# Kernel tuning notes

Hardware: AMD Instinct MI355X
Metric: run time of the kernel (lower is better)

Reference implementation:

```python
import jax, jax.numpy as jnp
import numpy as np

B, T, D = 2, 2048, 1024
H, KVH = 16, 4
HD = D // H            # 64
HALF = HD // 2         # 32
DFF = 4096
KW = 15
EPS = 1e-6


def zcrms(x, scale):
    # zero-centred RMSNorm: (1 + scale) * x / rms(x)
    rms = jnp.sqrt(jnp.mean(jnp.square(x.astype(jnp.float32)), axis=-1, keepdims=True) + EPS)
    return ((1.0 + scale) * x / rms).astype(x.dtype)


def apply_rope(x, cos, sin):
    # x: [B, H, T, HD]; cos/sin: [T, HALF]
    c = cos[None, None, :, :]
    s = sin[None, None, :, :]
    x1, x2 = x[..., :HALF], x[..., HALF:]
    return jnp.concatenate([x1 * c - x2 * s, x2 * c + x1 * s], axis=-1)


def setup_inputs() -> dict:
    key = jax.random.key(0)
    ks = jax.random.split(key, 20)
    std = 0.02
    inp = {
        "x": jax.random.normal(ks[0], (B, T, D), jnp.float32),
        "mask": jnp.ones((1, 1, T, T), dtype=bool),
        "cos": jnp.cos(jnp.arange(T, dtype=jnp.float32)[:, None]
                       * (10000.0 ** (-jnp.arange(HALF, dtype=jnp.float32) / HALF))[None, :]),
        "sin": jnp.sin(jnp.arange(T, dtype=jnp.float32)[:, None]
                       * (10000.0 ** (-jnp.arange(HALF, dtype=jnp.float32) / HALF))[None, :]),
        # attention
        "attn_norm_scale": jax.random.normal(ks[1], (D,), jnp.float32) * std,
        "q_kernel": jax.random.normal(ks[2], (D, D), jnp.float32) * std,
        "k_kernel": jax.random.normal(ks[3], (D, KVH * HD), jnp.float32) * std,
        "v_kernel": jax.random.normal(ks[4], (D, KVH * HD), jnp.float32) * std,
        "q_norm_scale": jax.random.normal(ks[5], (HD,), jnp.float32) * std,
        "k_norm_scale": jax.random.normal(ks[6], (HD,), jnp.float32) * std,
        "o_kernel": jax.random.normal(ks[7], (D, D), jnp.float32) * std,
        # conv module
        "conv_norm_scale": jax.random.normal(ks[8], (D,), jnp.float32) * std,
        "pw_up_kernel": jax.random.normal(ks[9], (D, 2 * D), jnp.float32) * std,
        "dw_kernel": jax.random.normal(ks[10], (KW, 1, D), jnp.float32) * std,
        "conv_inner_norm_scale": jax.random.normal(ks[11], (D,), jnp.float32) * std,
        "pw_down_kernel": jax.random.normal(ks[12], (D, D), jnp.float32) * std,
        # ffn
        "ffn_norm_scale": jax.random.normal(ks[13], (D,), jnp.float32) * std,
        "gate_kernel": jax.random.normal(ks[14], (D, DFF), jnp.float32) * std,
        "up_kernel": jax.random.normal(ks[15], (D, DFF), jnp.float32) * std,
        "down_kernel": jax.random.normal(ks[16], (DFF, D), jnp.float32) * std,
    }
    return inp


def reference(x, mask, cos, sin, attn_norm_scale, q_kernel, k_kernel, v_kernel,
              q_norm_scale, k_norm_scale, o_kernel, conv_norm_scale, pw_up_kernel,
              dw_kernel, conv_inner_norm_scale, pw_down_kernel, ffn_norm_scale,
              gate_kernel, up_kernel, down_kernel):
    # ---- pre-norm self-attention (GQA + QK-RMSNorm + RoPE) ----
    h = zcrms(x, attn_norm_scale)
    q = (h @ q_kernel).reshape(B, T, H, HD).transpose(0, 2, 1, 3)      # [B,H,T,HD]
    k = (h @ k_kernel).reshape(B, T, KVH, HD).transpose(0, 2, 1, 3)    # [B,KVH,T,HD]
    v = (h @ v_kernel).reshape(B, T, KVH, HD).transpose(0, 2, 1, 3)
    q = zcrms(q, q_norm_scale)
    k = zcrms(k, k_norm_scale)
    rep = H // KVH
    k = jnp.repeat(k, rep, axis=1)
    v = jnp.repeat(v, rep, axis=1)
    q = apply_rope(q, cos, sin)
    k = apply_rope(k, cos, sin)
    scale = jnp.sqrt(jnp.float32(HD))
    aw = jnp.einsum('bhqd,bhkd->bhqk', q, k) / scale
    aw = jnp.where(mask, aw, jnp.finfo(aw.dtype).min)
    aw = jax.nn.softmax(aw, axis=-1)
    attn = jnp.einsum('bhqk,bhkd->bhqd', aw, v).transpose(0, 2, 1, 3).reshape(B, T, D)
    x = x + attn @ o_kernel

    # ---- conformer conv module: pw_up -> GLU -> depthwise conv -> norm -> pw_down ----
    h = zcrms(x, conv_norm_scale)
    u = h @ pw_up_kernel
    u1, u2 = jnp.split(u, 2, axis=-1)
    g = u1 * jax.nn.sigmoid(u2)                                        # [B,T,D]
    c = jax.lax.conv_general_dilated(
        g, dw_kernel, window_strides=(1,), padding='SAME',
        feature_group_count=D, dimension_numbers=('NWC', 'WIO', 'NWC'))
    c = zcrms(c, conv_inner_norm_scale)
    x = x + c @ pw_down_kernel

    # ---- gated FFN with drelu activation ----
    h = zcrms(x, ffn_norm_scale)
    ff = jax.nn.relu(h @ gate_kernel) * jax.nn.relu(h @ up_kernel)
    x = x + ff @ down_kernel
    return x
```

## Files before the change

kernel.cpp:

```cpp
#include <hip/hip_runtime.h>


#define TT   2048
#define NTOK 4096

typedef __attribute__((ext_vector_type(8))) short short8;
typedef __attribute__((ext_vector_type(4))) float floatx4;

__device__ __forceinline__ unsigned short f2bf(float f) {
  unsigned int u = __float_as_uint(f);
  u = (u + 0x7fffu + ((u >> 16) & 1u)) >> 16;
  return (unsigned short)u;
}
__device__ __forceinline__ float bf2f(unsigned short s) {
  return __uint_as_float(((unsigned int)s) << 16);
}

__device__ __forceinline__ void glds16(const void* g, void* lds_base) {
  __builtin_amdgcn_global_load_lds(
      (const __attribute__((address_space(1))) void*)g,
      (__attribute__((address_space(3))) void*)lds_base, 16, 0, 0);
}

struct WJobs {
  const float* src[9];
  unsigned short* dst[9];
  int K[9], M[9], pm[9];
  int start[10];
};

__global__ __launch_bounds__(256) void wconv_all_kernel(WJobs tab) {
  int b = blockIdx.x;
  int j = 0;
  while (b >= tab.start[j + 1]) j++;
  int t = b - tab.start[j];
  const float* src = tab.src[j];
  unsigned short* dst = tab.dst[j];
  int K = tab.K[j], M = tab.M[j], pm = tab.pm[j];
  int mt = M >> 5;
  int m0 = (t % mt) * 32, k0 = (t / mt) * 32;
  int rowbase;
  if (pm == 0)      rowbase = m0;
  else if (pm == 1) rowbase = ((m0 & 1023) >> 5) * 64 + (m0 >> 10) * 32;
  else if (pm == 2) rowbase = (m0 >> 5) * 64;
  else              rowbase = (m0 >> 5) * 64 + 32;
  __shared__ float tile[32][33];
  int tx = threadIdx.x & 31, ty = threadIdx.x >> 5;
  for (int r = ty; r < 32; r += 8)
    tile[r][tx] = src[(size_t)(k0 + r) * M + m0 + tx];
  __syncthreads();
  for (int r = ty; r < 32; r += 8)
    dst[(size_t)(rowbase + r) * K + k0 + tx] = f2bf(tile[tx][r]);
}

__global__ __launch_bounds__(256) void rmsnorm_kernel(
    const float* __restrict__ x, const float* __restrict__ scale,
    unsigned short* __restrict__ out) {
  int t = blockIdx.x, tid = threadIdx.x;
  float4 xv = ((const float4*)(x + (size_t)t * 1024))[tid];
  float ss = xv.x * xv.x + xv.y * xv.y + xv.z * xv.z + xv.w * xv.w;
#pragma unroll
  for (int off = 32; off > 0; off >>= 1) ss += __shfl_down(ss, off);
  __shared__ float red[4];
  if ((tid & 63) == 0) red[tid >> 6] = ss;
  __syncthreads();
  float rinv = rsqrtf((red[0] + red[1] + red[2] + red[3]) * (1.0f / 1024.0f) + 1e-6f);
  float4 sv = ((const float4*)scale)[tid];
  ushort4 o;
  o.x = f2bf((1.0f + sv.x) * xv.x * rinv);
  o.y = f2bf((1.0f + sv.y) * xv.y * rinv);
  o.z = f2bf((1.0f + sv.z) * xv.z * rinv);
  o.w = f2bf((1.0f + sv.w) * xv.w * rinv);
  ((ushort4*)(out + (size_t)t * 1024))[tid] = o;
}

template <int BN, int FUSE, bool OUT_BF16, bool RELU, bool RESID>
__global__ __launch_bounds__(256, 2) void gemm_bt_kernel(
    const unsigned short* __restrict__ A, const unsigned short* __restrict__ Bt,
    void* __restrict__ Cout, const float* __restrict__ resid, int K, int M) {
  constexpr int NI = BN / 32;
  __shared__ __align__(16) unsigned short As[128 * 64];
  __shared__ __align__(16) unsigned short Bs[BN * 64];
  const int tid = threadIdx.x;
  const int wid = tid >> 6, lane = tid & 63;
  const int quad = lane >> 4, l16 = lane & 15;
  const int wm = (wid >> 1) * 64, wn = (wid & 1) * (BN / 2);
  const int row0 = blockIdx.y * 128;
  const int col0 = blockIdx.x * BN;

  floatx4 acc[4][NI];
#pragma unroll
  for (int mi = 0; mi < 4; mi++)
#pragma unroll
    for (int ni = 0; ni < NI; ni++) acc[mi][ni] = (floatx4){0.f, 0.f, 0.f, 0.f};

  const unsigned short* Ag = A + (size_t)row0 * K;
  const unsigned short* Bg = Bt + (size_t)col0 * K;

  for (int k0 = 0; k0 < K; k0 += 64) {
#pragma unroll
    for (int j = 0; j < 4; j++) {
      int ci = tid + j * 256;
      int r = ci >> 3, c = (ci & 7) ^ (r & 7);
      glds16(Ag + (size_t)r * K + k0 + c * 8, &As[(wid * 64 + j * 256) * 8]);
    }
#pragma unroll
    for (int j = 0; j < BN / 32; j++) {
      int ci = tid + j * 256;
      int r = ci >> 3, c = (ci & 7) ^ (r & 7);
      glds16(Bg + (size_t)r * K + k0 + c * 8, &Bs[(wid * 64 + j * 256) * 8]);
    }
    __syncthreads();
#pragma unroll
    for (int kk = 0; kk < 64; kk += 32) {
      short8 a[4], b[NI];
#pragma unroll
      for (int mi = 0; mi < 4; mi++) {
        int r = wm + mi * 16 + l16;
        a[mi] = *(const short8*)&As[r * 64 + (((kk >> 3) + quad) ^ (r & 7)) * 8];
      }
#pragma unroll
      for (int ni = 0; ni < NI; ni++) {
        int r = wn + ni * 16 + l16;
        b[ni] = *(const short8*)&Bs[r * 64 + (((kk >> 3) + quad) ^ (r & 7)) * 8];
      }
#pragma unroll
      for (int mi = 0; mi < 4; mi++)
#pragma unroll
        for (int ni = 0; ni < NI; ni++)
          acc[mi][ni] = __builtin_amdgcn_mfma_f32_16x16x32_bf16(a[mi], b[ni], acc[mi][ni], 0, 0, 0);
    }
    __syncthreads();
  }

  if (FUSE == 0) {
#pragma unroll
    for (int mi = 0; mi < 4; mi++) {
#pragma unroll
      for (int reg = 0; reg < 4; reg++) {
        int grow = row0 + wm + mi * 16 + quad * 4 + reg;
#pragma unroll
        for (int ni = 0; ni < NI; ni++) {
          int gcol = col0 + wn + ni * 16 + l16;
          float v = acc[mi][ni][reg];
          if (RESID) v += resid[(size_t)grow * M + gcol];
          if (RELU) v = fmaxf(v, 0.f);
          if (OUT_BF16) ((unsigned short*)Cout)[(size_t)grow * M + gcol] = f2bf(v);
          else          ((float*)Cout)[(size_t)grow * M + gcol] = v;
        }
      }
    }
  } else {
    const int group = (col0 + wn) >> 6;
    const int MW = M >> 1;
#pragma unroll
    for (int mi = 0; mi < 4; mi++) {
#pragma unroll
      for (int reg = 0; reg < 4; reg++) {
        int grow = row0 + wm + mi * 16 + quad * 4 + reg;
#pragma unroll
        for (int ni = 0; ni < NI / 2; ni++) {
          int f = group * 32 + ni * 16 + l16;
          float a = acc[mi][ni][reg], b = acc[mi][ni + NI / 2][reg];
          float v;
          if (FUSE == 1) v = a / (1.0f + __expf(-b));
          else           v = fmaxf(a, 0.f) * fmaxf(b, 0.f);
          ((unsigned short*)Cout)[(size_t)grow * MW + f] = f2bf(v);
        }
      }
    }
  }
}

#define QSCALE 0.180336880111f

__global__ __launch_bounds__(256) void qknorm_rope_kernel(
    const unsigned short* __restrict__ qkv, const float* __restrict__ cosb,
    const float* __restrict__ sinb, const float* __restrict__ qns,
    const float* __restrict__ kns, unsigned short* __restrict__ qb,
    unsigned short* __restrict__ kb, unsigned short* __restrict__ vb) {
  int tok = blockIdx.x;
  int tid = threadIdx.x, w = tid >> 6, lane = tid & 63;
  int pos = tok & (TT - 1);
  int half = lane & 31;
  float c = cosb[pos * 32 + half], s = sinb[pos * 32 + half];
  const unsigned short* row = qkv + (size_t)tok * 1536;
  for (int hr = w; hr < 20; hr += 4) {
    float v = bf2f(row[hr * 64 + lane]);
    float ss = v * v;
#pragma unroll
    for (int off = 32; off > 0; off >>= 1) ss += __shfl_xor(ss, off);
    float rinv = rsqrtf(ss * (1.0f / 64.0f) + 1e-6f);
    float sc = (hr < 16) ? qns[lane] : kns[lane];
    float nv = (1.0f + sc) * v * rinv;
    float partner = __shfl_xor(nv, 32);
    float outv = (lane < 32) ? (nv * c - partner * s) : (nv * c + partner * s);
    if (hr < 16) qb[(size_t)tok * 1024 + hr * 64 + lane] = f2bf(outv * QSCALE);
    else         kb[(size_t)tok * 256 + (hr - 16) * 64 + lane] = f2bf(outv);
  }
  vb[(size_t)tok * 256 + tid] = row[1280 + tid];
}

__global__ __launch_bounds__(256) void vtrans_kernel(
    const unsigned short* __restrict__ vb, unsigned short* __restrict__ vt) {
  __shared__ unsigned short t[64 * 65];
  int ktile = blockIdx.x;
  int g = blockIdx.y;
  int bi = g >> 2, kvh = g & 3;
  int tid = threadIdx.x;
#pragma unroll
  for (int j = 0; j < 2; j++) {
    int ci = tid + j * 256;
    int r = ci >> 3, c8 = (ci & 7) * 8;
    union { uint4 v; unsigned short u[8]; } uu;
    uu.v = *(const uint4*)(vb + (size_t)(bi * TT + ktile * 64 + r) * 256 + kvh * 64 + c8);
#pragma unroll
    for (int e = 0; e < 8; e++) t[r * 65 + c8 + e] = uu.u[e];
  }
  __syncthreads();
#pragma unroll
  for (int j = 0; j < 2; j++) {
    int ci = tid + j * 256;
    int d = ci >> 3, c8 = (ci & 7) * 8;
    union { uint4 v; unsigned short u[8]; } uu;
#pragma unroll
    for (int e = 0; e < 8; e++) uu.u[e] = t[(c8 + e) * 65 + d];
    *(uint4*)(vt + ((size_t)(g * 64 + d)) * TT + ktile * 64 + c8) = uu.v;
  }
}

__global__ __launch_bounds__(256) void flash_kernel(
    const unsigned short* __restrict__ qb, const unsigned short* __restrict__ kb,
    const unsigned short* __restrict__ vt, unsigned short* __restrict__ ob) {
  const int qt = blockIdx.x;
  const int bh = blockIdx.y;
  const int bi = bh >> 4, h = bh & 15, kvh = h >> 2;
  const int tid = threadIdx.x, w = tid >> 6, lane = tid & 63;
  const int quad = lane >> 4, l16 = lane & 15;

  __shared__ __align__(16) unsigned short Ks[2][64 * 64];
  __shared__ __align__(16) unsigned short Vs[2][64 * 64];
  __shared__ __align__(16) unsigned short Ps[128 * 72];

  const unsigned short* qsrc = qb + ((size_t)(bi * TT + qt * 128)) * 1024 + h * 64;
  short8 qf[2][2];
#pragma unroll
  for (int af = 0; af < 2; af++) {
    const unsigned short* qr = qsrc + (size_t)(w * 32 + af * 16 + l16) * 1024;
    qf[af][0] = *(const short8*)(qr + quad * 8);
    qf[af][1] = *(const short8*)(qr + 32 + quad * 8);
  }

  const unsigned short* kbase = kb + ((size_t)(bi * TT)) * 256 + kvh * 64;
  const unsigned short* vbase = vt + ((size_t)(bi * 4 + kvh)) * (64 * TT);

  floatx4 oacc[2][4];
  floatx4 lacc[2];
#pragma unroll
  for (int af = 0; af < 2; af++) {
    lacc[af] = (floatx4){0.f, 0.f, 0.f, 0.f};
#pragma unroll
    for (int di = 0; di < 4; di++) oacc[af][di] = (floatx4){0.f, 0.f, 0.f, 0.f};
  }
  const short8 ones = (short8){0x3F80, 0x3F80, 0x3F80, 0x3F80,
                               0x3F80, 0x3F80, 0x3F80, 0x3F80};

#pragma unroll
  for (int j = 0; j < 2; j++) {
    int ci = tid + j * 256;
    int r = ci >> 3, c = (ci & 7) ^ (r & 7);
    glds16(kbase + (size_t)r * 256 + c * 8, &Ks[0][(w * 64 + j * 256) * 8]);
    glds16(vbase + (size_t)r * TT + c * 8, &Vs[0][(w * 64 + j * 256) * 8]);
  }

  for (int kt = 0; kt < 32; kt++) {
    const int buf = kt & 1;
    __syncthreads();
    if (kt < 31) {
#pragma unroll
      for (int j = 0; j < 2; j++) {
        int ci = tid + j * 256;
        int r = ci >> 3, c = (ci & 7) ^ (r & 7);
        glds16(kbase + (size_t)((kt + 1) * 64 + r) * 256 + c * 8,
               &Ks[buf ^ 1][(w * 64 + j * 256) * 8]);
        glds16(vbase + (size_t)r * TT + (kt + 1) * 64 + c * 8,
               &Vs[buf ^ 1][(w * 64 + j * 256) * 8]);
      }
    }

    short8 kf[4][2];
#pragma unroll
    for (int ni = 0; ni < 4; ni++) {
      int rb = ni * 16 + l16;
      kf[ni][0] = *(const short8*)&Ks[buf][rb * 64 + ((quad ^ (rb & 7)) * 8)];
      kf[ni][1] = *(const short8*)&Ks[buf][rb * 64 + (((4 + quad) ^ (rb & 7)) * 8)];
    }
#pragma unroll
    for (int af = 0; af < 2; af++) {
#pragma unroll
      for (int ni = 0; ni < 4; ni++) {
        floatx4 s = (floatx4){0.f, 0.f, 0.f, 0.f};
        s = __builtin_amdgcn_mfma_f32_16x16x32_bf16(qf[af][0], kf[ni][0], s, 0, 0, 0);
        s = __builtin_amdgcn_mfma_f32_16x16x32_bf16(qf[af][1], kf[ni][1], s, 0, 0, 0);
#pragma unroll
        for (int r = 0; r < 4; r++)
          Ps[(w * 32 + af * 16 + quad * 4 + r) * 72 + ((ni ^ quad) * 16 + l16)] =
              (unsigned short)(__float_as_uint(__builtin_amdgcn_exp2f(s[r])) >> 16);
      }
    }
    short8 vf[4][2];
#pragma unroll
    for (int di = 0; di < 4; di++) {
      int rb = di * 16 + l16;
      vf[di][0] = *(const short8*)&Vs[buf][rb * 64 + ((quad ^ (rb & 7)) * 8)];
      vf[di][1] = *(const short8*)&Vs[buf][rb * 64 + (((4 + quad) ^ (rb & 7)) * 8)];
    }
#pragma unroll
    for (int af = 0; af < 2; af++) {
      const int rr = w * 32 + af * 16 + l16;
      const int sw = l16 >> 2;
      short8 pa0 = *(const short8*)&Ps[rr * 72 + (((quad >> 1) ^ sw) * 16 + (quad & 1) * 8)];
      short8 pa1 = *(const short8*)&Ps[rr * 72 + ((((quad >> 1) + 2) ^ sw) * 16 + (quad & 1) * 8)];
      lacc[af] = __builtin_amdgcn_mfma_f32_16x16x32_bf16(pa0, ones, lacc[af], 0, 0, 0);
      lacc[af] = __builtin_amdgcn_mfma_f32_16x16x32_bf16(pa1, ones, lacc[af], 0, 0, 0);
#pragma unroll
      for (int di = 0; di < 4; di++) {
        oacc[af][di] = __builtin_amdgcn_mfma_f32_16x16x32_bf16(pa0, vf[di][0], oacc[af][di], 0, 0, 0);
        oacc[af][di] = __builtin_amdgcn_mfma_f32_16x16x32_bf16(pa1, vf[di][1], oacc[af][di], 0, 0, 0);
      }
    }
  }

  unsigned short* obase = ob + ((size_t)(bi * TT + qt * 128)) * 1024 + h * 64;
#pragma unroll
  for (int af = 0; af < 2; af++) {
    float rl[4];
#pragma unroll
    for (int r = 0; r < 4; r++) rl[r] = 1.0f / lacc[af][r];
#pragma unroll
    for (int di = 0; di < 4; di++)
#pragma unroll
      for (int r = 0; r < 4; r++) {
        int qrow = w * 32 + af * 16 + quad * 4 + r;
        obase[(size_t)qrow * 1024 + di * 16 + l16] = f2bf(oacc[af][di][r] * rl[r]);
      }
  }
}

__global__ __launch_bounds__(256) void convnorm_kernel(
    const unsigned short* __restrict__ g, const float* __restrict__ dw,
    const float* __restrict__ scale, unsigned short* __restrict__ out) {
  int tok = blockIdx.x;
  int bi = tok >> 11, pos = tok & (TT - 1);
  int tid = threadIdx.x, c0 = tid * 4;
  float a0 = 0.f, a1 = 0.f, a2 = 0.f, a3 = 0.f;
#pragma unroll
  for (int wk = 0; wk < 15; wk++) {
    int pp = pos + wk - 7;
    if (pp < 0 || pp >= TT) continue;
    ushort4 gv = *(const ushort4*)(g + ((size_t)(bi * TT + pp)) * 1024 + c0);
    float4 kv = *(const float4*)(dw + wk * 1024 + c0);
    a0 += bf2f(gv.x) * kv.x;
    a1 += bf2f(gv.y) * kv.y;
    a2 += bf2f(gv.z) * kv.z;
    a3 += bf2f(gv.w) * kv.w;
  }
  float ss = a0 * a0 + a1 * a1 + a2 * a2 + a3 * a3;
#pragma unroll
  for (int off = 32; off > 0; off >>= 1) ss += __shfl_down(ss, off);
  __shared__ float red[4];
  if ((tid & 63) == 0) red[tid >> 6] = ss;
  __syncthreads();
  float rinv = rsqrtf((red[0] + red[1] + red[2] + red[3]) * (1.0f / 1024.0f) + 1e-6f);
  float4 sv = *(const float4*)(scale + c0);
  ushort4 o;
  o.x = f2bf((1.0f + sv.x) * a0 * rinv);
  o.y = f2bf((1.0f + sv.y) * a1 * rinv);
  o.z = f2bf((1.0f + sv.z) * a2 * rinv);
  o.w = f2bf((1.0f + sv.w) * a3 * rinv);
  *(ushort4*)(out + (size_t)tok * 1024 + c0) = o;
}

extern "C" void kernel_launch(void* const* d_in, const int* in_sizes, int n_in,
                              void* d_out, int out_size, void* d_ws, size_t ws_size,
                              hipStream_t stream) {
  const float* x        = (const float*)d_in[0];
  const float* cosb     = (const float*)d_in[2];
  const float* sinb     = (const float*)d_in[3];
  const float* attn_ns  = (const float*)d_in[4];
  const float* qkern    = (const float*)d_in[5];
  const float* kkern    = (const float*)d_in[6];
  const float* vkern    = (const float*)d_in[7];
  const float* qns      = (const float*)d_in[8];
  const float* kns      = (const float*)d_in[9];
  const float* okern    = (const float*)d_in[10];
  const float* conv_ns  = (const float*)d_in[11];
  const float* pwupk    = (const float*)d_in[12];
  const float* dwk      = (const float*)d_in[13];
  const float* convi_ns = (const float*)d_in[14];
  const float* pwdnk    = (const float*)d_in[15];
  const float* ffn_ns   = (const float*)d_in[16];
  const float* gatek    = (const float*)d_in[17];
  const float* upk      = (const float*)d_in[18];
  const float* downk    = (const float*)d_in[19];
  float* out = (float*)d_out;
  char* ws = (char*)d_ws;

  const size_t O_QKVT = 0;
  const size_t O_OT   = O_QKVT + (size_t)1536 * 1024 * 2;
  const size_t O_UPT  = O_OT   + (size_t)1024 * 1024 * 2;
  const size_t O_DNT  = O_UPT  + (size_t)2048 * 1024 * 2;
  const size_t O_GUT  = O_DNT  + (size_t)1024 * 1024 * 2;
  const size_t O_DWNT = O_GUT  + (size_t)8192 * 1024 * 2;
  const size_t O_H    = O_DWNT + (size_t)4096 * 1024 * 2;
  const size_t O_BIG1 = O_H    + (size_t)4096 * 1024 * 2;
  const size_t O_QB   = O_BIG1 + (size_t)4096 * 8192 * 2;
  const size_t O_KB   = O_QB   + (size_t)4096 * 1024 * 2;
  const size_t O_VB   = O_KB   + (size_t)4096 * 256 * 2;
  const size_t O_VT   = O_VB   + (size_t)4096 * 256 * 2;
  const size_t O_ECN  = O_VT   + (size_t)8 * 64 * 2048 * 2;
  const size_t O_X1   = O_ECN  + (size_t)4096 * 1024 * 2;
  const size_t O_X2   = O_X1   + (size_t)4096 * 1024 * 4;
  const size_t O_BIG2 = O_X2   + (size_t)4096 * 1024 * 4;

  unsigned short* qkvT = (unsigned short*)(ws + O_QKVT);
  unsigned short* oT   = (unsigned short*)(ws + O_OT);
  unsigned short* upT  = (unsigned short*)(ws + O_UPT);
  unsigned short* dnT  = (unsigned short*)(ws + O_DNT);
  unsigned short* guT  = (unsigned short*)(ws + O_GUT);
  unsigned short* dwT  = (unsigned short*)(ws + O_DWNT);
  unsigned short* hbuf = (unsigned short*)(ws + O_H);
  unsigned short* big1u = (unsigned short*)(ws + O_BIG1);
  unsigned short* qbuf = (unsigned short*)(ws + O_QB);
  unsigned short* kbuf = (unsigned short*)(ws + O_KB);
  unsigned short* vbuf = (unsigned short*)(ws + O_VB);
  unsigned short* vtb  = (unsigned short*)(ws + O_VT);
  unsigned short* ecn  = (unsigned short*)(ws + O_ECN);
  float*          x1   = (float*)(ws + O_X1);
  float*          x2   = (float*)(ws + O_X2);
  unsigned short* big2 = (unsigned short*)(ws + O_BIG2);

  WJobs tab;
  tab.src[0] = qkern;  tab.dst[0] = qkvT;                       tab.K[0] = 1024; tab.M[0] = 1024; tab.pm[0] = 0;
  tab.src[1] = kkern;  tab.dst[1] = qkvT + (size_t)1024 * 1024; tab.K[1] = 1024; tab.M[1] = 256;  tab.pm[1] = 0;
  tab.src[2] = vkern;  tab.dst[2] = qkvT + (size_t)1280 * 1024; tab.K[2] = 1024; tab.M[2] = 256;  tab.pm[2] = 0;
  tab.src[3] = okern;  tab.dst[3] = oT;                         tab.K[3] = 1024; tab.M[3] = 1024; tab.pm[3] = 0;
  tab.src[4] = pwupk;  tab.dst[4] = upT;                        tab.K[4] = 1024; tab.M[4] = 2048; tab.pm[4] = 1;
  tab.src[5] = pwdnk;  tab.dst[5] = dnT;                        tab.K[5] = 1024; tab.M[5] = 1024; tab.pm[5] = 0;
  tab.src[6] = gatek;  tab.dst[6] = guT;                        tab.K[6] = 1024; tab.M[6] = 4096; tab.pm[6] = 2;
  tab.src[7] = upk;    tab.dst[7] = guT;                        tab.K[7] = 1024; tab.M[7] = 4096; tab.pm[7] = 3;
  tab.src[8] = downk;  tab.dst[8] = dwT;                        tab.K[8] = 4096; tab.M[8] = 1024; tab.pm[8] = 0;
  tab.start[0] = 0;
  for (int i = 0; i < 9; i++)
    tab.start[i + 1] = tab.start[i] + (tab.M[i] >> 5) * (tab.K[i] >> 5);
  wconv_all_kernel<<<tab.start[9], 256, 0, stream>>>(tab);

  rmsnorm_kernel<<<NTOK, 256, 0, stream>>>(x, attn_ns, hbuf);
  gemm_bt_kernel<128, 0, true, false, false><<<dim3(12, 32), 256, 0, stream>>>(
      hbuf, qkvT, big1u, nullptr, 1024, 1536);
  qknorm_rope_kernel<<<NTOK, 256, 0, stream>>>(big1u, cosb, sinb, qns, kns,
                                               qbuf, kbuf, vbuf);
  vtrans_kernel<<<dim3(32, 8), 256, 0, stream>>>(vbuf, vtb);
  flash_kernel<<<dim3(16, 32), 256, 0, stream>>>(qbuf, kbuf, vtb, ecn);
  gemm_bt_kernel<64, 0, false, false, true><<<dim3(16, 32), 256, 0, stream>>>(
      ecn, oT, x1, x, 1024, 1024);

  rmsnorm_kernel<<<NTOK, 256, 0, stream>>>(x1, conv_ns, hbuf);
  gemm_bt_kernel<128, 1, false, false, false><<<dim3(16, 32), 256, 0, stream>>>(
      hbuf, upT, big2, nullptr, 1024, 2048);
  convnorm_kernel<<<NTOK, 256, 0, stream>>>(big2, dwk, convi_ns, ecn);
  gemm_bt_kernel<64, 0, false, false, true><<<dim3(16, 32), 256, 0, stream>>>(
      ecn, dnT, x2, x1, 1024, 1024);

  rmsnorm_kernel<<<NTOK, 256, 0, stream>>>(x2, ffn_ns, hbuf);
  gemm_bt_kernel<128, 2, false, false, false><<<dim3(64, 32), 256, 0, stream>>>(
      hbuf, guT, big1u, nullptr, 1024, 8192);
  gemm_bt_kernel<64, 0, false, false, true><<<dim3(16, 32), 256, 0, stream>>>(
      big1u, dwT, out, x2, 4096, 1024);
}
```

Baseline: 484.9 us.

## Store residual stream in bf16, read V directly, and double flash block size

Intermediate residual activations x1 and x2 are now stored as bf16 instead of fp32. The rmsnorm and GEMM epilogues are templated to read bf16 input or residual, which halves that traffic at a precision cost. The separate V copy out of the QKV buffer is removed, and vtrans now reads V directly from the QKV output. The flash attention kernel moves to 512 threads and 256-row query tiles with a new XOR-swizzled P layout, so each K/V tile is shared by more queries. The grid shrinks from 512 to 256 blocks, which may reduce occupancy.

```diff
diff --git a/kernel.cpp b/kernel.cpp
--- a/kernel.cpp
+++ b/kernel.cpp
@@ -53,12 +53,20 @@
     dst[(size_t)(rowbase + r) * K + k0 + tx] = f2bf(tile[tx][r]);
 }
 
+template <bool BF16IN>
 __global__ __launch_bounds__(256) void rmsnorm_kernel(
-    const float* __restrict__ x, const float* __restrict__ scale,
+    const void* __restrict__ xin, const float* __restrict__ scale,
     unsigned short* __restrict__ out) {
   int t = blockIdx.x, tid = threadIdx.x;
-  float4 xv = ((const float4*)(x + (size_t)t * 1024))[tid];
-  float ss = xv.x * xv.x + xv.y * xv.y + xv.z * xv.z + xv.w * xv.w;
+  float xv[4];
+  if (BF16IN) {
+    ushort4 u = ((const ushort4*)((const unsigned short*)xin + (size_t)t * 1024))[tid];
+    xv[0] = bf2f(u.x); xv[1] = bf2f(u.y); xv[2] = bf2f(u.z); xv[3] = bf2f(u.w);
+  } else {
+    float4 u = ((const float4*)((const float*)xin + (size_t)t * 1024))[tid];
+    xv[0] = u.x; xv[1] = u.y; xv[2] = u.z; xv[3] = u.w;
+  }
+  float ss = xv[0] * xv[0] + xv[1] * xv[1] + xv[2] * xv[2] + xv[3] * xv[3];
 #pragma unroll
   for (int off = 32; off > 0; off >>= 1) ss += __shfl_down(ss, off);
   __shared__ float red[4];
@@ -67,17 +75,17 @@
   float rinv = rsqrtf((red[0] + red[1] + red[2] + red[3]) * (1.0f / 1024.0f) + 1e-6f);
   float4 sv = ((const float4*)scale)[tid];
   ushort4 o;
-  o.x = f2bf((1.0f + sv.x) * xv.x * rinv);
-  o.y = f2bf((1.0f + sv.y) * xv.y * rinv);
-  o.z = f2bf((1.0f + sv.z) * xv.z * rinv);
-  o.w = f2bf((1.0f + sv.w) * xv.w * rinv);
+  o.x = f2bf((1.0f + sv.x) * xv[0] * rinv);
+  o.y = f2bf((1.0f + sv.y) * xv[1] * rinv);
+  o.z = f2bf((1.0f + sv.z) * xv[2] * rinv);
+  o.w = f2bf((1.0f + sv.w) * xv[3] * rinv);
   ((ushort4*)(out + (size_t)t * 1024))[tid] = o;
 }
 
-template <int BN, int FUSE, bool OUT_BF16, bool RELU, bool RESID>
+template <int BN, int FUSE, int OUT, int RES>
 __global__ __launch_bounds__(256, 2) void gemm_bt_kernel(
     const unsigned short* __restrict__ A, const unsigned short* __restrict__ Bt,
-    void* __restrict__ Cout, const float* __restrict__ resid, int K, int M) {
+    void* __restrict__ Cout, const void* __restrict__ resid, int K, int M) {
   constexpr int NI = BN / 32;
   __shared__ __align__(16) unsigned short As[128 * 64];
   __shared__ __align__(16) unsigned short Bs[BN * 64];
@@ -143,9 +151,9 @@
         for (int ni = 0; ni < NI; ni++) {
           int gcol = col0 + wn + ni * 16 + l16;
           float v = acc[mi][ni][reg];
-          if (RESID) v += resid[(size_t)grow * M + gcol];
-          if (RELU) v = fmaxf(v, 0.f);
-          if (OUT_BF16) ((unsigned short*)Cout)[(size_t)grow * M + gcol] = f2bf(v);
+          if (RES == 1) v += ((const float*)resid)[(size_t)grow * M + gcol];
+          if (RES == 2) v += bf2f(((const unsigned short*)resid)[(size_t)grow * M + gcol]);
+          if (OUT == 1) ((unsigned short*)Cout)[(size_t)grow * M + gcol] = f2bf(v);
           else          ((float*)Cout)[(size_t)grow * M + gcol] = v;
         }
       }
@@ -178,7 +186,7 @@
     const unsigned short* __restrict__ qkv, const float* __restrict__ cosb,
     const float* __restrict__ sinb, const float* __restrict__ qns,
     const float* __restrict__ kns, unsigned short* __restrict__ qb,
-    unsigned short* __restrict__ kb, unsigned short* __restrict__ vb) {
+    unsigned short* __restrict__ kb) {
   int tok = blockIdx.x;
   int tid = threadIdx.x, w = tid >> 6, lane = tid & 63;
   int pos = tok & (TT - 1);
@@ -198,11 +206,10 @@
     if (hr < 16) qb[(size_t)tok * 1024 + hr * 64 + lane] = f2bf(outv * QSCALE);
     else         kb[(size_t)tok * 256 + (hr - 16) * 64 + lane] = f2bf(outv);
   }
-  vb[(size_t)tok * 256 + tid] = row[1280 + tid];
 }
 
 __global__ __launch_bounds__(256) void vtrans_kernel(
-    const unsigned short* __restrict__ vb, unsigned short* __restrict__ vt) {
+    const unsigned short* __restrict__ qkv, unsigned short* __restrict__ vt) {
   __shared__ unsigned short t[64 * 65];
   int ktile = blockIdx.x;
   int g = blockIdx.y;
@@ -213,7 +220,8 @@
     int ci = tid + j * 256;
     int r = ci >> 3, c8 = (ci & 7) * 8;
     union { uint4 v; unsigned short u[8]; } uu;
-    uu.v = *(const uint4*)(vb + (size_t)(bi * TT + ktile * 64 + r) * 256 + kvh * 64 + c8);
+    uu.v = *(const uint4*)(qkv + (size_t)(bi * TT + ktile * 64 + r) * 1536 +
+                           1280 + kvh * 64 + c8);
 #pragma unroll
     for (int e = 0; e < 8; e++) t[r * 65 + c8 + e] = uu.u[e];
   }
@@ -229,7 +237,7 @@
   }
 }
 
-__global__ __launch_bounds__(256) void flash_kernel(
+__global__ __launch_bounds__(512) void flash_kernel(
     const unsigned short* __restrict__ qb, const unsigned short* __restrict__ kb,
     const unsigned short* __restrict__ vt, unsigned short* __restrict__ ob) {
   const int qt = blockIdx.x;
@@ -240,9 +248,9 @@
 
   __shared__ __align__(16) unsigned short Ks[2][64 * 64];
   __shared__ __align__(16) unsigned short Vs[2][64 * 64];
-  __shared__ __align__(16) unsigned short Ps[128 * 72];
-
-  const unsigned short* qsrc = qb + ((size_t)(bi * TT + qt * 128)) * 1024 + h * 64;
+  __shared__ __align__(16) unsigned short Ps[256 * 64];
+
+  const unsigned short* qsrc = qb + ((size_t)(bi * TT + qt * 256)) * 1024 + h * 64;
   short8 qf[2][2];
 #pragma unroll
   for (int af = 0; af < 2; af++) {
@@ -265,27 +273,19 @@
   const short8 ones = (short8){0x3F80, 0x3F80, 0x3F80, 0x3F80,
                                0x3F80, 0x3F80, 0x3F80, 0x3F80};
 
-#pragma unroll
-  for (int j = 0; j < 2; j++) {
-    int ci = tid + j * 256;
-    int r = ci >> 3, c = (ci & 7) ^ (r & 7);
-    glds16(kbase + (size_t)r * 256 + c * 8, &Ks[0][(w * 64 + j * 256) * 8]);
-    glds16(vbase + (size_t)r * TT + c * 8, &Vs[0][(w * 64 + j * 256) * 8]);
+  {
+    int r = tid >> 3, c = (tid & 7) ^ (r & 7);
+    glds16(kbase + (size_t)r * 256 + c * 8, &Ks[0][w * 512]);
+    glds16(vbase + (size_t)r * TT + c * 8, &Vs[0][w * 512]);
   }
 
   for (int kt = 0; kt < 32; kt++) {
     const int buf = kt & 1;
     __syncthreads();
     if (kt < 31) {
-#pragma unroll
-      for (int j = 0; j < 2; j++) {
-        int ci = tid + j * 256;
-        int r = ci >> 3, c = (ci & 7) ^ (r & 7);
-        glds16(kbase + (size_t)((kt + 1) * 64 + r) * 256 + c * 8,
-               &Ks[buf ^ 1][(w * 64 + j * 256) * 8]);
-        glds16(vbase + (size_t)r * TT + (kt + 1) * 64 + c * 8,
-               &Vs[buf ^ 1][(w * 64 + j * 256) * 8]);
-      }
+      int r = tid >> 3, c = (tid & 7) ^ (r & 7);
+      glds16(kbase + (size_t)((kt + 1) * 64 + r) * 256 + c * 8, &Ks[buf ^ 1][w * 512]);
+      glds16(vbase + (size_t)r * TT + (kt + 1) * 64 + c * 8, &Vs[buf ^ 1][w * 512]);
     }
 
     short8 kf[4][2];
@@ -303,9 +303,12 @@
         s = __builtin_amdgcn_mfma_f32_16x16x32_bf16(qf[af][0], kf[ni][0], s, 0, 0, 0);
         s = __builtin_amdgcn_mfma_f32_16x16x32_bf16(qf[af][1], kf[ni][1], s, 0, 0, 0);
 #pragma unroll
-        for (int r = 0; r < 4; r++)
-          Ps[(w * 32 + af * 16 + quad * 4 + r) * 72 + ((ni ^ quad) * 16 + l16)] =
+        for (int r = 0; r < 4; r++) {
+          int rr = w * 32 + af * 16 + quad * 4 + r;
+          int ch = (ni * 2 + (l16 >> 3)) ^ (rr & 7);
+          Ps[rr * 64 + ch * 8 + (l16 & 7)] =
               (unsigned short)(__float_as_uint(__builtin_amdgcn_exp2f(s[r])) >> 16);
+        }
       }
     }
     short8 vf[4][2];
@@ -318,9 +321,8 @@
 #pragma unroll
     for (int af = 0; af < 2; af++) {
       const int rr = w * 32 + af * 16 + l16;
-      const int sw = l16 >> 2;
-      short8 pa0 = *(const short8*)&Ps[rr * 72 + (((quad >> 1) ^ sw) * 16 + (quad & 1) * 8)];
-      short8 pa1 = *(const short8*)&Ps[rr * 72 + ((((quad >> 1) + 2) ^ sw) * 16 + (quad & 1) * 8)];
+      short8 pa0 = *(const short8*)&Ps[rr * 64 + ((quad ^ (rr & 7)) * 8)];
+      short8 pa1 = *(const short8*)&Ps[rr * 64 + (((4 + quad) ^ (rr & 7)) * 8)];
       lacc[af] = __builtin_amdgcn_mfma_f32_16x16x32_bf16(pa0, ones, lacc[af], 0, 0, 0);
       lacc[af] = __builtin_amdgcn_mfma_f32_16x16x32_bf16(pa1, ones, lacc[af], 0, 0, 0);
 #pragma unroll
@@ -331,7 +333,7 @@
     }
   }
 
-  unsigned short* obase = ob + ((size_t)(bi * TT + qt * 128)) * 1024 + h * 64;
+  unsigned short* obase = ob + ((size_t)(bi * TT + qt * 256)) * 1024 + h * 64;
 #pragma unroll
   for (int af = 0; af < 2; af++) {
     float rl[4];
@@ -416,12 +418,11 @@
   const size_t O_BIG1 = O_H    + (size_t)4096 * 1024 * 2;
   const size_t O_QB   = O_BIG1 + (size_t)4096 * 8192 * 2;
   const size_t O_KB   = O_QB   + (size_t)4096 * 1024 * 2;
-  const size_t O_VB   = O_KB   + (size_t)4096 * 256 * 2;
-  const size_t O_VT   = O_VB   + (size_t)4096 * 256 * 2;
+  const size_t O_VT   = O_KB   + (size_t)4096 * 256 * 2;
   const size_t O_ECN  = O_VT   + (size_t)8 * 64 * 2048 * 2;
   const size_t O_X1   = O_ECN  + (size_t)4096 * 1024 * 2;
-  const size_t O_X2   = O_X1   + (size_t)4096 * 1024 * 4;
-  const size_t O_BIG2 = O_X2   + (size_t)4096 * 1024 * 4;
+  const size_t O_X2   = O_X1   + (size_t)4096 * 1024 * 2;
+  const size_t O_BIG2 = O_X2   + (size_t)4096 * 1024 * 2;
 
   unsigned short* qkvT = (unsigned short*)(ws + O_QKVT);
   unsigned short* oT   = (unsigned short*)(ws + O_OT);
@@ -433,11 +434,10 @@
   unsigned short* big1u = (unsigned short*)(ws + O_BIG1);
   unsigned short* qbuf = (unsigned short*)(ws + O_QB);
   unsigned short* kbuf = (unsigned short*)(ws + O_KB);
-  unsigned short* vbuf = (unsigned short*)(ws + O_VB);
   unsigned short* vtb  = (unsigned short*)(ws + O_VT);
   unsigned short* ecn  = (unsigned short*)(ws + O_ECN);
-  float*          x1   = (float*)(ws + O_X1);
-  float*          x2   = (float*)(ws + O_X2);
+  unsigned short* x1b  = (unsigned short*)(ws + O_X1);
+  unsigned short* x2b  = (unsigned short*)(ws + O_X2);
   unsigned short* big2 = (unsigned short*)(ws + O_BIG2);
 
   WJobs tab;
@@ -455,26 +455,26 @@
     tab.start[i + 1] = tab.start[i] + (tab.M[i] >> 5) * (tab.K[i] >> 5);
   wconv_all_kernel<<<tab.start[9], 256, 0, stream>>>(tab);
 
-  rmsnorm_kernel<<<NTOK, 256, 0, stream>>>(x, attn_ns, hbuf);
-  gemm_bt_kernel<128, 0, true, false, false><<<dim3(12, 32), 256, 0, stream>>>(
+  rmsnorm_kernel<false><<<NTOK, 256, 0, stream>>>(x, attn_ns, hbuf);
+  gemm_bt_kernel<128, 0, 1, 0><<<dim3(12, 32), 256, 0, stream>>>(
       hbuf, qkvT, big1u, nullptr, 1024, 1536);
   qknorm_rope_kernel<<<NTOK, 256, 0, stream>>>(big1u, cosb, sinb, qns, kns,
-                                               qbuf, kbuf, vbuf);
-  vtrans_kernel<<<dim3(32, 8), 256, 0, stream>>>(vbuf, vtb);
-  flash_kernel<<<dim3(16, 32), 256, 0, stream>>>(qbuf, kbuf, vtb, ecn);
-  gemm_bt_kernel<64, 0, false, false, true><<<dim3(16, 32), 256, 0, stream>>>(
-      ecn, oT, x1, x, 1024, 1024);
-
-  rmsnorm_kernel<<<NTOK, 256, 0, stream>>>(x1, conv_ns, hbuf);
-  gemm_bt_kernel<128, 1, false, false, false><<<dim3(16, 32), 256, 0, stream>>>(
+                                               qbuf, kbuf);
+  vtrans_kernel<<<dim3(32, 8), 256, 0, stream>>>(big1u, vtb);
+  flash_kernel<<<dim3(8, 32), 512, 0, stream>>>(qbuf, kbuf, vtb, ecn);
+  gemm_bt_kernel<64, 0, 1, 1><<<dim3(16, 32), 256, 0, stream>>>(
+      ecn, oT, x1b, x, 1024, 1024);
+
+  rmsnorm_kernel<true><<<NTOK, 256, 0, stream>>>(x1b, conv_ns, hbuf);
+  gemm_bt_kernel<128, 1, 1, 0><<<dim3(16, 32), 256, 0, stream>>>(
       hbuf, upT, big2, nullptr, 1024, 2048);
   convnorm_kernel<<<NTOK, 256, 0, stream>>>(big2, dwk, convi_ns, ecn);
-  gemm_bt_kernel<64, 0, false, false, true><<<dim3(16, 32), 256, 0, stream>>>(
-      ecn, dnT, x2, x1, 1024, 1024);
-
-  rmsnorm_kernel<<<NTOK, 256, 0, stream>>>(x2, ffn_ns, hbuf);
-  gemm_bt_kernel<128, 2, false, false, false><<<dim3(64, 32), 256, 0, stream>>>(
+  gemm_bt_kernel<64, 0, 1, 2><<<dim3(16, 32), 256, 0, stream>>>(
+      ecn, dnT, x2b, x1b, 1024, 1024);
+
+  rmsnorm_kernel<true><<<NTOK, 256, 0, stream>>>(x2b, ffn_ns, hbuf);
+  gemm_bt_kernel<128, 2, 1, 0><<<dim3(64, 32), 256, 0, stream>>>(
       hbuf, guT, big1u, nullptr, 1024, 8192);
-  gemm_bt_kernel<64, 0, false, false, true><<<dim3(16, 32), 256, 0, stream>>>(
-      big1u, dwT, out, x2, 4096, 1024);
-}
+  gemm_bt_kernel<64, 0, 0, 2><<<dim3(16, 32), 256, 0, stream>>>(
+      big1u, dwT, out, x2b, 4096, 1024);
+}
```

After: 488.6 us. Within noise of the previous version (+0.8%).
